# Optimization experiments

Measured on AMD Instinct MI355X. Metric: run time of the kernel, lower is better.

Reference implementation:

```python
import jax, jax.numpy as jnp
import numpy as np

D_K = 64
SCALE = 1.0 / np.sqrt(D_K).astype(np.float32)
NEG_INF = -1e9


def setup_inputs() -> dict:
    key = jax.random.key(0)
    kq, kk, kv, km = jax.random.split(key, 4)
    B, H, S, D = 2, 16, 2048, D_K
    Q = jax.random.normal(kq, (B, H, S, D), dtype=jnp.float32)
    K = jax.random.normal(kk, (B, H, S, D), dtype=jnp.float32)
    V = jax.random.normal(kv, (B, H, S, D), dtype=jnp.float32)
    atten_mask = jax.random.randint(km, (B, H, S, S), 0, 2, dtype=jnp.int32)
    return {"Q": Q, "K": K, "V": V, "atten_mask": atten_mask}


def reference(Q, K, V, atten_mask):
    # scores: [B, H, Sq, Sk]
    scores = jnp.einsum("bhqd,bhkd->bhqk", Q, K) * SCALE
    scores = jnp.where(atten_mask.astype(bool), NEG_INF, scores)
    weights = jax.nn.softmax(scores, axis=-1)
    context = jnp.einsum("bhqk,bhkd->bhqd", weights, V)
    return (context, weights)
```

## Files before the change

kernel.cpp:

```cpp
#include <hip/hip_runtime.h>


#define S_LEN 2048
#define D_HEAD 64
#define BM 32
#define BN 64
#define NKB (S_LEN / BN)
#define CTX_ELEMS (2 * 16 * 2048 * 64)

typedef __attribute__((ext_vector_type(4))) float f32x4;
typedef __attribute__((ext_vector_type(8))) __bf16 bf16x8;
typedef __attribute__((ext_vector_type(2))) __bf16 bf16x2;

__device__ __forceinline__ bf16x8 pack8(f32x4 a, f32x4 b, float sc) {
    bf16x8 r;
    r[0] = (__bf16)(a[0] * sc); r[1] = (__bf16)(a[1] * sc);
    r[2] = (__bf16)(a[2] * sc); r[3] = (__bf16)(a[3] * sc);
    r[4] = (__bf16)(b[0] * sc); r[5] = (__bf16)(b[1] * sc);
    r[6] = (__bf16)(b[2] * sc); r[7] = (__bf16)(b[7 - 7] * sc);
    r[6] = (__bf16)(b[2] * sc); r[7] = (__bf16)(b[3] * sc);
    return r;
}

#define MFMA16(a, b, c) __builtin_amdgcn_mfma_f32_16x16x32_bf16(a, b, c, 0, 0, 0)

struct PF1 {
    f32x4 v[4];
    f32x4 k[4];
    int   m[8];
};
struct PF2 {
    f32x4 k[4];
};


__global__ __launch_bounds__(256, 4) void attn_fwd(
    const float* __restrict__ Qg, const float* __restrict__ Kg,
    const float* __restrict__ Vg, const int* __restrict__ Mg,
    float* __restrict__ outg)
{
    __shared__ __align__(16) __bf16 Vt[2][64][72];
    __shared__ __align__(16) __bf16 Pb[2][32][72];
    __shared__ unsigned short bmap[32][128];
    __shared__ float redl[4][32];
    __shared__ float invl[32];

    const int tid  = threadIdx.x;
    const int wave = tid >> 6;
    const int lane = tid & 63;
    const int c    = lane & 15;
    const int quad = lane >> 4;

    const int bid  = blockIdx.x;
    const int bh   = bid >> 6;
    const int row0 = (bid & 63) * BM;

    const float* Qh = Qg + (size_t)bh * S_LEN * D_HEAD;
    const float* Kh = Kg + (size_t)bh * S_LEN * D_HEAD;
    const float* Vh = Vg + (size_t)bh * S_LEN * D_HEAD;
    const int*   Mh = Mg + ((size_t)bh * S_LEN + row0) * S_LEN;
    float* ctx  = outg + ((size_t)bh * S_LEN + row0) * D_HEAD;
    float* wout = outg + (size_t)CTX_ELEMS + ((size_t)bh * S_LEN + row0) * S_LEN;

    bf16x8 aQ[2][2];
    #pragma unroll
    for (int t = 0; t < 2; ++t)
      #pragma unroll
      for (int h = 0; h < 2; ++h) {
        const float* p = Qh + (size_t)(row0 + 16 * t + c) * D_HEAD + 32 * h + quad * 8;
        aQ[t][h] = pack8(*(const f32x4*)p, *(const f32x4*)(p + 4), 0.125f);
      }

    f32x4 accO[2];
    accO[0] = (f32x4){0.f, 0.f, 0.f, 0.f};
    accO[1] = (f32x4){0.f, 0.f, 0.f, 0.f};
    float lacc[2][4] = {{0.f,0.f,0.f,0.f},{0.f,0.f,0.f,0.f}};

    const int vk2 = (tid & 31) * 2;
    const int vd8 = (tid >> 5) * 8;

#define ISSUE_V(P, KN) {                                                      \
    const float* vp_ = Vh + (size_t)((KN) * BN + vk2) * D_HEAD + vd8;         \
    (P).v[0] = *(const f32x4*)vp_;                                            \
    (P).v[1] = *(const f32x4*)(vp_ + 4);                                      \
    (P).v[2] = *(const f32x4*)(vp_ + D_HEAD);                                 \
    (P).v[3] = *(const f32x4*)(vp_ + D_HEAD + 4); }

#define ISSUE_K(P, KN) {                                                      \
    const float* kp_ = Kh + (size_t)((KN) * BN + 16 * wave + c) * D_HEAD + quad * 8; \
    (P).k[0] = *(const f32x4*)kp_;                                            \
    (P).k[1] = *(const f32x4*)(kp_ + 4);                                      \
    (P).k[2] = *(const f32x4*)(kp_ + 32);                                     \
    (P).k[3] = *(const f32x4*)(kp_ + 36); }

#define ISSUE_M(P, KN) {                                                      \
    const int* mp_ = Mh + (KN) * BN + 16 * wave + c;                          \
    _Pragma("unroll")                                                         \
    for (int t_ = 0; t_ < 2; ++t_)                                            \
      _Pragma("unroll")                                                       \
      for (int r_ = 0; r_ < 4; ++r_)                                          \
        (P).m[4 * t_ + r_] =                                                  \
            __builtin_nontemporal_load(mp_ + (size_t)(16 * t_ + 4 * quad + r_) * S_LEN); }

#define LDS_BARRIER() {                                                       \
    asm volatile("s_waitcnt lgkmcnt(0)" ::: "memory");                        \
    __builtin_amdgcn_s_barrier(); }

#define P1BODY(KB, CUR, NXT) {                                                \
    const int kn_ = ((KB) + 1 < NKB) ? (KB) + 1 : (KB);                       \
        \
    _Pragma("unroll")                                                         \
    for (int i_ = 0; i_ < 4; ++i_) {                                          \
        bf16x2 p0_; p0_[0] = (__bf16)CUR.v[0][i_]; p0_[1] = (__bf16)CUR.v[2][i_]; \
        *(bf16x2*)&Vt[buf][vd8 + i_][vk2] = p0_;                              \
        bf16x2 p1_; p1_[0] = (__bf16)CUR.v[1][i_]; p1_[1] = (__bf16)CUR.v[3][i_]; \
        *(bf16x2*)&Vt[buf][vd8 + 4 + i_][vk2] = p1_;                          \
    }                                                                         \
    ISSUE_V(NXT, kn_);                                                        \
                     \
    bf16x8 bK0_ = pack8(CUR.k[0], CUR.k[1], 1.0f);                            \
    bf16x8 bK1_ = pack8(CUR.k[2], CUR.k[3], 1.0f);                            \
    ISSUE_K(NXT, kn_);                                                        \
    f32x4 sc0_ = (f32x4){0.f, 0.f, 0.f, 0.f};                                 \
    f32x4 sc1_ = (f32x4){0.f, 0.f, 0.f, 0.f};                                 \
    sc0_ = MFMA16(aQ[0][0], bK0_, sc0_);                                      \
    sc1_ = MFMA16(aQ[1][0], bK0_, sc1_);                                      \
    sc0_ = MFMA16(aQ[0][1], bK1_, sc0_);                                      \
    sc1_ = MFMA16(aQ[1][1], bK1_, sc1_);                                      \
     \
    _Pragma("unroll")                                                         \
    for (int t_ = 0; t_ < 2; ++t_)                                            \
      _Pragma("unroll")                                                       \
      for (int r_ = 0; r_ < 4; ++r_) {                                        \
        const int lrow_ = 16 * t_ + 4 * quad + r_;                            \
        const int mv_   = CUR.m[4 * t_ + r_];                                 \
        const unsigned long long bal_ = __ballot(mv_ != 0);                   \
        const float sv_ = (t_ == 0) ? sc0_[r_] : sc1_[r_];                    \
        const float pv_ = mv_ ? 0.f : __expf(sv_);                            \
        lacc[t_][r_] += pv_;                                                  \
        Pb[buf][lrow_][16 * wave + c] = (__bf16)pv_;                          \
        if (c == 0)                                                           \
            bmap[lrow_][4 * (KB) + wave] = (unsigned short)(bal_ >> (16 * quad)); \
      }                                                                       \
    ISSUE_M(NXT, kn_);                                                        \
    LDS_BARRIER();                                                            \
            \
    _Pragma("unroll")                                                         \
    for (int h_ = 0; h_ < 2; ++h_) {                                          \
        bf16x8 bV_  = *(const bf16x8*)&Vt[buf][16 * wave + c][32 * h_ + quad * 8]; \
        bf16x8 aP0_ = *(const bf16x8*)&Pb[buf][c][32 * h_ + quad * 8];        \
        bf16x8 aP1_ = *(const bf16x8*)&Pb[buf][16 + c][32 * h_ + quad * 8];   \
        accO[0] = MFMA16(aP0_, bV_, accO[0]);                                 \
        accO[1] = MFMA16(aP1_, bV_, accO[1]);                                 \
    }                                                                         \
    buf ^= 1; }

    int buf = 0;
    PF1 pf0, pf1;
    ISSUE_V(pf0, 0);
    ISSUE_K(pf0, 0);
    ISSUE_M(pf0, 0);
    for (int kb = 0; kb < NKB; kb += 2) {
        P1BODY(kb,     pf0, pf1);
        P1BODY(kb + 1, pf1, pf0);
    }

    #pragma unroll
    for (int t = 0; t < 2; ++t)
      #pragma unroll
      for (int r = 0; r < 4; ++r) {
        float v = lacc[t][r];
        v += __shfl_xor(v, 1);
        v += __shfl_xor(v, 2);
        v += __shfl_xor(v, 4);
        v += __shfl_xor(v, 8);
        lacc[t][r] = v;
      }
    if (c == 0) {
        #pragma unroll
        for (int t = 0; t < 2; ++t)
          #pragma unroll
          for (int r = 0; r < 4; ++r)
            redl[wave][16 * t + 4 * quad + r] = lacc[t][r];
    }
    __syncthreads();
    if (tid < 32) {
        float s = redl[0][tid] + redl[1][tid] + redl[2][tid] + redl[3][tid];
        invl[tid] = 1.0f / s;
    }
    __syncthreads();

    float inv[2][4];
    #pragma unroll
    for (int t = 0; t < 2; ++t)
      #pragma unroll
      for (int r = 0; r < 4; ++r)
        inv[t][r] = invl[16 * t + 4 * quad + r];

    #pragma unroll
    for (int t = 0; t < 2; ++t)
      #pragma unroll
      for (int r = 0; r < 4; ++r)
        ctx[(size_t)(16 * t + 4 * quad + r) * D_HEAD + 16 * wave + c] = accO[t][r] * inv[t][r];

#define P2BODY(KB, CUR, NXT) {                                                \
    const int kn_ = ((KB) + 1 < NKB) ? (KB) + 1 : (KB);                       \
    ISSUE_K(NXT, kn_);                                                        \
    bf16x8 bK0_ = pack8(CUR.k[0], CUR.k[1], 1.0f);                            \
    bf16x8 bK1_ = pack8(CUR.k[2], CUR.k[3], 1.0f);                            \
    f32x4 sc0_ = (f32x4){0.f, 0.f, 0.f, 0.f};                                 \
    f32x4 sc1_ = (f32x4){0.f, 0.f, 0.f, 0.f};                                 \
    sc0_ = MFMA16(aQ[0][0], bK0_, sc0_);                                      \
    sc1_ = MFMA16(aQ[1][0], bK0_, sc1_);                                      \
    sc0_ = MFMA16(aQ[0][1], bK1_, sc0_);                                      \
    sc1_ = MFMA16(aQ[1][1], bK1_, sc1_);                                      \
    const int k0_ = (KB) * BN;                                                \
    _Pragma("unroll")                                                         \
    for (int t_ = 0; t_ < 2; ++t_)                                            \
      _Pragma("unroll")                                                       \
      for (int r_ = 0; r_ < 4; ++r_) {                                        \
        const int lrow_ = 16 * t_ + 4 * quad + r_;                            \
        const unsigned bits_ = bmap[lrow_][4 * (KB) + wave];                  \
        const float sv_ = (t_ == 0) ? sc0_[r_] : sc1_[r_];                    \
        const float pv_ = ((bits_ >> c) & 1u) ? 0.f : __expf(sv_) * inv[t_][r_]; \
        __builtin_nontemporal_store(pv_, wout + (size_t)lrow_ * S_LEN + k0_ + 16 * wave + c); \
      } }

    PF2 qf0, qf1;
    ISSUE_K(qf0, 0);
    for (int kb = 0; kb < NKB; kb += 2) {
        P2BODY(kb,     qf0, qf1);
        P2BODY(kb + 1, qf1, qf0);
    }
}

extern "C" void kernel_launch(void* const* d_in, const int* in_sizes, int n_in,
                              void* d_out, int out_size, void* d_ws, size_t ws_size,
                              hipStream_t stream) {
    const float* Q = (const float*)d_in[0];
    const float* K = (const float*)d_in[1];
    const float* V = (const float*)d_in[2];
    const int*   M = (const int*)d_in[3];
    float* out = (float*)d_out;
    dim3 grid(2048);
    dim3 block(256);
    attn_fwd<<<grid, block, 0, stream>>>(Q, K, V, M, out);
}
```

Baseline: 1.282 ms.

## Preload attention mask as ballot bitmap upfront with vectorized loads, swizzle block order

```diff
diff --git a/kernel.cpp b/kernel.cpp
--- a/kernel.cpp
+++ b/kernel.cpp
@@ -9,6 +9,7 @@
 #define CTX_ELEMS (2 * 16 * 2048 * 64)
 
 typedef __attribute__((ext_vector_type(4))) float f32x4;
+typedef __attribute__((ext_vector_type(4))) int   i32x4;
 typedef __attribute__((ext_vector_type(8))) __bf16 bf16x8;
 typedef __attribute__((ext_vector_type(2))) __bf16 bf16x2;
 
@@ -17,7 +18,6 @@
     r[0] = (__bf16)(a[0] * sc); r[1] = (__bf16)(a[1] * sc);
     r[2] = (__bf16)(a[2] * sc); r[3] = (__bf16)(a[3] * sc);
     r[4] = (__bf16)(b[0] * sc); r[5] = (__bf16)(b[1] * sc);
-    r[6] = (__bf16)(b[2] * sc); r[7] = (__bf16)(b[7 - 7] * sc);
     r[6] = (__bf16)(b[2] * sc); r[7] = (__bf16)(b[3] * sc);
     return r;
 }
@@ -27,7 +27,6 @@
 struct PF1 {
     f32x4 v[4];
     f32x4 k[4];
-    int   m[8];
 };
 struct PF2 {
     f32x4 k[4];
@@ -41,7 +40,7 @@
 {
     __shared__ __align__(16) __bf16 Vt[2][64][72];
     __shared__ __align__(16) __bf16 Pb[2][32][72];
-    __shared__ unsigned short bmap[32][128];
+    __shared__ unsigned long long bst[32][32];
     __shared__ float redl[4][32];
     __shared__ float invl[32];
 
@@ -51,7 +50,7 @@
     const int c    = lane & 15;
     const int quad = lane >> 4;
 
-    const int bid  = blockIdx.x;
+    const int bid  = (blockIdx.x & 7) * (2048 / 8) + (blockIdx.x >> 3);
     const int bh   = bid >> 6;
     const int row0 = (bid & 63) * BM;
 
@@ -71,6 +70,23 @@
         aQ[t][h] = pack8(*(const f32x4*)p, *(const f32x4*)(p + 4), 0.125f);
       }
 
+    for (int s = 0; s < 64; ++s) {
+        const int mrow  = s >> 1;
+        const int cbase = ((s & 1) << 10) + (wave << 8);
+        const i32x4 mv4 = __builtin_nontemporal_load(
+            (const i32x4*)(Mh + (size_t)mrow * S_LEN + cbase + 4 * lane));
+        const unsigned long long b0 = __ballot(mv4[0] != 0);
+        const unsigned long long b1 = __ballot(mv4[1] != 0);
+        const unsigned long long b2 = __ballot(mv4[2] != 0);
+        const unsigned long long b3 = __ballot(mv4[3] != 0);
+        if (lane == 0) {
+            const int g4 = ((((s & 1) << 2) + wave) << 2);
+            bst[mrow][g4 + 0] = b0; bst[mrow][g4 + 1] = b1;
+            bst[mrow][g4 + 2] = b2; bst[mrow][g4 + 3] = b3;
+        }
+    }
+    __syncthreads();
+
     f32x4 accO[2];
     accO[0] = (f32x4){0.f, 0.f, 0.f, 0.f};
     accO[1] = (f32x4){0.f, 0.f, 0.f, 0.f};
@@ -93,21 +109,15 @@
     (P).k[2] = *(const f32x4*)(kp_ + 32);                                     \
     (P).k[3] = *(const f32x4*)(kp_ + 36); }
 
-#define ISSUE_M(P, KN) {                                                      \
-    const int* mp_ = Mh + (KN) * BN + 16 * wave + c;                          \
-    _Pragma("unroll")                                                         \
-    for (int t_ = 0; t_ < 2; ++t_)                                            \
-      _Pragma("unroll")                                                       \
-      for (int r_ = 0; r_ < 4; ++r_)                                          \
-        (P).m[4 * t_ + r_] =                                                  \
-            __builtin_nontemporal_load(mp_ + (size_t)(16 * t_ + 4 * quad + r_) * S_LEN); }
+#define GETBIT(LROW, KB)                                                      \
+    ((int)((bst[LROW][(((KB) >> 2) << 2) + (c & 3)] >>                        \
+            ((((KB) & 3) << 4) + (wave << 2) + (c >> 2))) & 1ull))
 
 #define LDS_BARRIER() {                                                       \
     asm volatile("s_waitcnt lgkmcnt(0)" ::: "memory");                        \
     __builtin_amdgcn_s_barrier(); }
 
 #define P1BODY(KB, CUR, NXT) {                                                \
-    const int kn_ = ((KB) + 1 < NKB) ? (KB) + 1 : (KB);                       \
         \
     _Pragma("unroll")                                                         \
     for (int i_ = 0; i_ < 4; ++i_) {                                          \
@@ -116,33 +126,29 @@
         bf16x2 p1_; p1_[0] = (__bf16)CUR.v[1][i_]; p1_[1] = (__bf16)CUR.v[3][i_]; \
         *(bf16x2*)&Vt[buf][vd8 + 4 + i_][vk2] = p1_;                          \
     }                                                                         \
-    ISSUE_V(NXT, kn_);                                                        \
+    if ((KB) + 1 < NKB) ISSUE_V(NXT, (KB) + 1);                               \
                      \
     bf16x8 bK0_ = pack8(CUR.k[0], CUR.k[1], 1.0f);                            \
     bf16x8 bK1_ = pack8(CUR.k[2], CUR.k[3], 1.0f);                            \
-    ISSUE_K(NXT, kn_);                                                        \
+    if ((KB) + 1 < NKB) ISSUE_K(NXT, (KB) + 1);                               \
     f32x4 sc0_ = (f32x4){0.f, 0.f, 0.f, 0.f};                                 \
     f32x4 sc1_ = (f32x4){0.f, 0.f, 0.f, 0.f};                                 \
     sc0_ = MFMA16(aQ[0][0], bK0_, sc0_);                                      \
     sc1_ = MFMA16(aQ[1][0], bK0_, sc1_);                                      \
     sc0_ = MFMA16(aQ[0][1], bK1_, sc0_);                                      \
     sc1_ = MFMA16(aQ[1][1], bK1_, sc1_);                                      \
-     \
+       \
     _Pragma("unroll")                                                         \
     for (int t_ = 0; t_ < 2; ++t_)                                            \
       _Pragma("unroll")                                                       \
       for (int r_ = 0; r_ < 4; ++r_) {                                        \
         const int lrow_ = 16 * t_ + 4 * quad + r_;                            \
-        const int mv_   = CUR.m[4 * t_ + r_];                                 \
-        const unsigned long long bal_ = __ballot(mv_ != 0);                   \
+        const int mv_   = GETBIT(lrow_, (KB));                                \
         const float sv_ = (t_ == 0) ? sc0_[r_] : sc1_[r_];                    \
         const float pv_ = mv_ ? 0.f : __expf(sv_);                            \
         lacc[t_][r_] += pv_;                                                  \
         Pb[buf][lrow_][16 * wave + c] = (__bf16)pv_;                          \
-        if (c == 0)                                                           \
-            bmap[lrow_][4 * (KB) + wave] = (unsigned short)(bal_ >> (16 * quad)); \
       }                                                                       \
-    ISSUE_M(NXT, kn_);                                                        \
     LDS_BARRIER();                                                            \
             \
     _Pragma("unroll")                                                         \
@@ -159,7 +165,6 @@
     PF1 pf0, pf1;
     ISSUE_V(pf0, 0);
     ISSUE_K(pf0, 0);
-    ISSUE_M(pf0, 0);
     for (int kb = 0; kb < NKB; kb += 2) {
         P1BODY(kb,     pf0, pf1);
         P1BODY(kb + 1, pf1, pf0);
@@ -204,8 +209,7 @@
         ctx[(size_t)(16 * t + 4 * quad + r) * D_HEAD + 16 * wave + c] = accO[t][r] * inv[t][r];
 
 #define P2BODY(KB, CUR, NXT) {                                                \
-    const int kn_ = ((KB) + 1 < NKB) ? (KB) + 1 : (KB);                       \
-    ISSUE_K(NXT, kn_);                                                        \
+    if ((KB) + 1 < NKB) ISSUE_K(NXT, (KB) + 1);                               \
     bf16x8 bK0_ = pack8(CUR.k[0], CUR.k[1], 1.0f);                            \
     bf16x8 bK1_ = pack8(CUR.k[2], CUR.k[3], 1.0f);                            \
     f32x4 sc0_ = (f32x4){0.f, 0.f, 0.f, 0.f};                                 \
@@ -220,10 +224,10 @@
       _Pragma("unroll")                                                       \
       for (int r_ = 0; r_ < 4; ++r_) {                                        \
         const int lrow_ = 16 * t_ + 4 * quad + r_;                            \
-        const unsigned bits_ = bmap[lrow_][4 * (KB) + wave];                  \
+        const int mv_   = GETBIT(lrow_, (KB));                                \
         const float sv_ = (t_ == 0) ? sc0_[r_] : sc1_[r_];                    \
-        const float pv_ = ((bits_ >> c) & 1u) ? 0.f : __expf(sv_) * inv[t_][r_]; \
-        __builtin_nontemporal_store(pv_, wout + (size_t)lrow_ * S_LEN + k0_ + 16 * wave + c); \
+        const float pv_ = mv_ ? 0.f : __expf(sv_) * inv[t_][r_];              \
+        wout[(size_t)lrow_ * S_LEN + k0_ + 16 * wave + c] = pv_;              \
       } }
 
     PF2 qf0, qf1;
```

Result: faster. 1.206 ms (-5.9%).
